# Performance work log

Measured on AMD Instinct MI355X. Metric: run time of the kernel, lower is better.

Reference implementation:

```python
import jax, jax.numpy as jnp
import numpy as np

B, C, D, H, W = 4, 256, 16, 16, 16
INTER = C // 8  # 32


def setup_inputs() -> dict:
    key = jax.random.key(0)
    ks = jax.random.split(key, 8)
    return {
        "x": jax.random.normal(ks[0], (B, C, D, H, W), dtype=jnp.float32),
        "Wq": jax.random.normal(ks[1], (INTER, C), dtype=jnp.float32) * 0.05,
        "bq": jax.random.normal(ks[2], (INTER,), dtype=jnp.float32) * 0.05,
        "Wk": jax.random.normal(ks[3], (INTER, C), dtype=jnp.float32) * 0.05,
        "bk": jax.random.normal(ks[4], (INTER,), dtype=jnp.float32) * 0.05,
        "Wv": jax.random.normal(ks[5], (C, C), dtype=jnp.float32) * 0.05,
        "bv": jax.random.normal(ks[6], (C,), dtype=jnp.float32) * 0.05,
        "gamma": jax.random.normal(ks[7], (1,), dtype=jnp.float32),
    }


def reference(x, Wq, bq, Wk, bk, Wv, bv, gamma):
    b, c, d, h, w = x.shape
    n = d * h * w
    xf = x.reshape(b, c, n)  # [B, C, N]
    # 1x1 Conv3d == pointwise channel projection
    q = jnp.einsum("oc,bcn->bon", Wq, xf) + bq[None, :, None]  # [B, inter, N]
    k = jnp.einsum("oc,bcn->bon", Wk, xf) + bk[None, :, None]  # [B, inter, N]
    v = jnp.einsum("oc,bcn->bon", Wv, xf) + bv[None, :, None]  # [B, C, N]
    scale = float(q.shape[1]) ** 0.5
    # attn[b, i, j] = <q[:, i], k[:, j]>
    attn = jax.nn.softmax(jnp.einsum("bci,bcj->bij", q, k) / scale, axis=-1)
    # out[b, c, i] = sum_j v[b, c, j] * attn[b, i, j]
    out = jnp.einsum("bcj,bij->bci", v, attn).reshape(b, c, d, h, w)
    return gamma[0] * out + x
```

## Files before the change

### kernel.cpp

```cpp
#include <hip/hip_runtime.h>

#define B_ 4
#define C_ 256
#define N_ 4096
#define INTER_ 32

typedef __attribute__((ext_vector_type(8))) short short8;
typedef __attribute__((ext_vector_type(4))) float f32x4;
typedef __attribute__((ext_vector_type(16))) float f32x16;
typedef __attribute__((ext_vector_type(4))) unsigned int u32x4;

#define TILEB 18432
#define NSTG  (8 * TILEB)

static __device__ __forceinline__ unsigned short f2bf(float f) {
    unsigned int u = __builtin_bit_cast(unsigned int, f);
    u += 0x7fff + ((u >> 16) & 1);
    return (unsigned short)(u >> 16);
}

static __device__ __forceinline__ unsigned int cvtpk(float lo, float hi) {
    unsigned int r;
    asm("v_cvt_pk_bf16_f32 %0, %1, %2" : "=v"(r) : "v"(lo), "v"(hi));
    return r;
}

static __device__ __forceinline__ void pl32swap(unsigned int& a, unsigned int& b) {
    asm("v_permlane32_swap_b32 %0, %1" : "+v"(a), "+v"(b));
}

static __device__ __forceinline__ float exp2a(float x) {
    float r;
    asm("v_exp_f32 %0, %1" : "=v"(r) : "v"(x));
    return r;
}

static __device__ __forceinline__ void gload16(const void* g, void* l) {
    __builtin_amdgcn_global_load_lds(
        (const __attribute__((address_space(1))) void*)g,
        (__attribute__((address_space(3))) void*)l, 16, 0, 0);
}

__global__ __launch_bounds__(256) void prep_kernel(
    const float* __restrict__ Wq, const float* __restrict__ Wk,
    const float* __restrict__ Wv, unsigned short* __restrict__ wb)
{
    int i = blockIdx.x * 256 + threadIdx.x;
    int row = i >> 8, col = i & 255;
    float v;
    if (row < 32)      v = Wq[row * 256 + col];
    else if (row < 64) v = Wk[(row - 32) * 256 + col];
    else               v = Wv[(row - 64) * 256 + col];
    wb[i] = f2bf(v);
}

__global__ __launch_bounds__(256) void qkv_kernel(
    const float* __restrict__ x, const unsigned short* __restrict__ wb,
    const float* __restrict__ bq, const float* __restrict__ bk,
    const float* __restrict__ bv,
    unsigned short* __restrict__ qb, unsigned short* __restrict__ kfrag,
    unsigned short* __restrict__ vfrag)
{
    const int tid  = threadIdx.x;
    const int wave = tid >> 6;
    const int lane = tid & 63;
    const int l31  = lane & 31;
    const int h2   = lane >> 5;
    const int b    = blockIdx.x >> 6;
    const int n0   = (blockIdx.x & 63) * 64;

    __shared__ unsigned int xsh[64 * 129];

    {
        const float* xb = x + ((size_t)b * C_ + 64 * wave) * N_ + n0 + lane;
        unsigned int* dst = xsh + (size_t)lane * 129 + 32 * wave;
        #pragma unroll 8
        for (int s = 0; s < 32; ++s) {
            float v0 = xb[(size_t)(2 * s) * N_];
            float v1 = xb[(size_t)(2 * s + 1) * N_];
            dst[s] = (unsigned int)f2bf(v0) | ((unsigned int)f2bf(v1) << 16);
        }
    }
    __syncthreads();

    const float rs = 0.25504183f;

    #pragma unroll
    for (int u = 0; u < 5; ++u) {
        const int unit = wave + 4 * u;
        const int ch = unit >> 1;
        const int ns = unit & 1;
        const int ncol = n0 + 32 * ns + l31;
        const int jt = (n0 >> 5) + ns;

        const float* bias = (ch == 0) ? bq : (ch == 1) ? bk : (bv + (ch - 2) * 32);
        f32x16 acc;
        #pragma unroll
        for (int r = 0; r < 16; ++r)
            acc[r] = bias[(r & 3) + 8 * (r >> 2) + 4 * h2];

        const unsigned short* wrow = wb + ((size_t)(ch * 32 + l31)) * 256 + 8 * h2;
        const unsigned int*   xrow = xsh + (size_t)(32 * ns + l31) * 129 + 4 * h2;

        #pragma unroll
        for (int kk = 0; kk < 16; ++kk) {
            short8 wa = *reinterpret_cast<const short8*>(wrow + 16 * kk);
            short8 xf = *reinterpret_cast<const short8*>(xrow + 8 * kk);
            acc = __builtin_amdgcn_mfma_f32_32x32x16_bf16(wa, xf, acc, 0, 0, 0);
        }

        if (ch == 0) {
            unsigned short* dst = qb + ((size_t)b * N_ + ncol) * 32;
            #pragma unroll
            for (int q = 0; q < 4; ++q) {
                unsigned int w0 = (unsigned int)f2bf(acc[4 * q] * rs)
                                | ((unsigned int)f2bf(acc[4 * q + 1] * rs) << 16);
                unsigned int w1 = (unsigned int)f2bf(acc[4 * q + 2] * rs)
                                | ((unsigned int)f2bf(acc[4 * q + 3] * rs) << 16);
                unsigned int* p = reinterpret_cast<unsigned int*>(dst + 4 * h2 + 8 * q);
                p[0] = w0; p[1] = w1;
            }
        } else if (ch == 1) {
            unsigned short* kt = kfrag + ((size_t)b * 128 + jt) * 1024;
            #pragma unroll
            for (int r = 0; r < 16; ++r) {
                const int co = (r & 3) + 8 * (r >> 2) + 4 * h2;
                const int addr = ((co >> 4) << 9) + ((l31 + 32 * ((co >> 3) & 1)) << 3)
                               + (co & 7);
                kt[addr] = f2bf(acc[r]);
            }
        } else {
            const int g = ch - 2;
            unsigned short* vt_ = vfrag + (((size_t)b * 128 + jt) * 8 + g) * 1024;
            #pragma unroll
            for (int r = 0; r < 16; ++r) {
                const int co = (r & 3) + 8 * (r >> 2) + 4 * h2;
                const int addr = ((l31 >> 4) << 9) + ((co + 32 * ((l31 >> 3) & 1)) << 3)
                               + (l31 & 7);
                vt_[addr] = f2bf(acc[r]);
            }
        }
    }
}

__global__ __launch_bounds__(512) void attn_kernel(
    const unsigned short* __restrict__ qb, const unsigned short* __restrict__ kfrag,
    const unsigned short* __restrict__ vfrag,
    const float* __restrict__ x, const float* __restrict__ gamma,
    float* __restrict__ out)
{
    const int tid  = threadIdx.x;
    const int wave = tid >> 6;
    const int lane = tid & 63;
    const int l31  = lane & 31;
    const int h2   = lane >> 5;
    const int jq   = wave >> 1;
    const int qs   = wave & 1;

    const int bid  = blockIdx.x;
    const int xcd  = bid & 7;
    const int slot = bid >> 3;
    const int b    = xcd >> 1;
    const int ib   = slot * 2 + (xcd & 1);
    const int iq   = ib * 64 + 32 * qs;

    __shared__ char lds[NSTG];
    __shared__ float m_sh[8][32];
    __shared__ float l_sh[8][32];

    const unsigned short* vtb = vfrag + (size_t)b * 128 * 8192;
    const unsigned short* ktb = kfrag + (size_t)b * 128 * 1024;

    char* reg0 = lds + (jq * 2) * TILEB;
    char* reg1 = reg0 + TILEB;

    short8 qf0 = *reinterpret_cast<const short8*>(
        qb + ((size_t)b * N_ + iq + l31) * 32 + 8 * h2);
    short8 qf1 = *reinterpret_cast<const short8*>(
        qb + ((size_t)b * N_ + iq + l31) * 32 + 8 * h2 + 16);

    f32x16 acc[8];
    #pragma unroll
    for (int g = 0; g < 8; ++g)
        #pragma unroll
        for (int r = 0; r < 16; ++r) acc[g][r] = 0.f;

    float m_run = 0.f;
    float l_run = 0.f;
    const f32x16 z16 = {};

    {
        const char* vs = (const char*)(vtb + (size_t)(jq * 32) * 8192);
        const char* ks = (const char*)(ktb + (size_t)(jq * 32) * 1024);
        #pragma unroll
        for (int s2 = 0; s2 < 9; ++s2) {
            const int off = qs * 9216 + s2 * 1024;
            const char* g = (off < 16384) ? (vs + off) : (ks + (off - 16384));
            gload16(g + lane * 16, reg0 + off);
        }
    }
    __syncthreads();

    #pragma unroll 1
    for (int t = 0; t < 32; ++t) {
        char* cur = (t & 1) ? reg1 : reg0;
        char* nxt = (t & 1) ? reg0 : reg1;

        if (t < 31) {
            const int jtg = jq * 32 + t + 1;
            const char* vs = (const char*)(vtb + (size_t)jtg * 8192);
            const char* ks = (const char*)(ktb + (size_t)jtg * 1024);
            #pragma unroll
            for (int s2 = 0; s2 < 9; ++s2) {
                const int off = qs * 9216 + s2 * 1024;
                const char* g = (off < 16384) ? (vs + off) : (ks + (off - 16384));
                gload16(g + lane * 16, nxt + off);
            }
        }

        const char* kt_ = cur + 16384;
        short8 ka0 = *reinterpret_cast<const short8*>(kt_ + lane * 16);
        short8 ka1 = *reinterpret_cast<const short8*>(kt_ + 1024 + lane * 16);
        f32x16 s = __builtin_amdgcn_mfma_f32_32x32x16_bf16(ka0, qf0, z16, 0, 0, 0);
        s = __builtin_amdgcn_mfma_f32_32x32x16_bf16(ka1, qf1, s, 0, 0, 0);

        float a0 = fmaxf(s[0], s[8]),  a1 = fmaxf(s[1], s[9]);
        float a2 = fmaxf(s[2], s[10]), a3 = fmaxf(s[3], s[11]);
        float a4 = fmaxf(s[4], s[12]), a5 = fmaxf(s[5], s[13]);
        float a6 = fmaxf(s[6], s[14]), a7 = fmaxf(s[7], s[15]);
        a0 = fmaxf(a0, a4); a1 = fmaxf(a1, a5); a2 = fmaxf(a2, a6); a3 = fmaxf(a3, a7);
        float smax = fmaxf(fmaxf(a0, a1), fmaxf(a2, a3));

        if (__any(smax > m_run + 8.0f)) {
            float sm2 = fmaxf(smax, __shfl_xor(smax, 32));
            float mnew = fmaxf(m_run, sm2);
            float corr = exp2a(m_run - mnew);
            m_run = mnew;
            l_run *= corr;
            #pragma unroll
            for (int g = 0; g < 8; ++g)
                #pragma unroll
                for (int r = 0; r < 16; ++r) acc[g][r] *= corr;
        }

        float p[16];
        float lsum = 0.f;
        #pragma unroll
        for (int r = 0; r < 16; ++r) { p[r] = exp2a(s[r] - m_run); lsum += p[r]; }
        l_run += lsum;

        unsigned int X0 = cvtpk(p[0],  p[1]),  X1 = cvtpk(p[2],  p[3]);
        unsigned int Y0 = cvtpk(p[4],  p[5]),  Y1 = cvtpk(p[6],  p[7]);
        unsigned int W0 = cvtpk(p[8],  p[9]),  W1 = cvtpk(p[10], p[11]);
        unsigned int V0 = cvtpk(p[12], p[13]), V1 = cvtpk(p[14], p[15]);
        pl32swap(X0, Y0); pl32swap(X1, Y1);
        pl32swap(W0, V0); pl32swap(W1, V1);
        short8 pb0 = __builtin_bit_cast(short8, u32x4{X0, X1, Y0, Y1});
        short8 pb1 = __builtin_bit_cast(short8, u32x4{W0, W1, V0, V1});

        __builtin_amdgcn_s_setprio(1);
        #pragma unroll
        for (int g = 0; g < 8; ++g) {
            short8 va0 = *reinterpret_cast<const short8*>(cur + g * 2048 + lane * 16);
            short8 va1 = *reinterpret_cast<const short8*>(cur + g * 2048 + 1024 + lane * 16);
            acc[g] = __builtin_amdgcn_mfma_f32_32x32x16_bf16(va0, pb0, acc[g], 0, 0, 0);
            acc[g] = __builtin_amdgcn_mfma_f32_32x32x16_bf16(va1, pb1, acc[g], 0, 0, 0);
        }
        __builtin_amdgcn_s_setprio(0);

        __syncthreads();
    }

    float l_tot = l_run + __shfl_xor(l_run, 32);
    if (lane < 32) { m_sh[wave][lane] = m_run; l_sh[wave][lane] = l_tot; }
    __syncthreads();

    float M = -1e30f, L = 0.f;
    #pragma unroll
    for (int w2 = 0; w2 < 4; ++w2) M = fmaxf(M, m_sh[w2 * 2 + qs][l31]);
    #pragma unroll
    for (int w2 = 0; w2 < 4; ++w2)
        L += exp2a(m_sh[w2 * 2 + qs][l31] - M) * l_sh[w2 * 2 + qs][l31];
    const float wgt = exp2a(m_run - M);
    #pragma unroll
    for (int g = 0; g < 8; ++g)
        #pragma unroll
        for (int r = 0; r < 16; ++r) acc[g][r] *= wgt;

    if (jq >= 2) {
        f32x4* Dr = (f32x4*)(lds + ((jq - 2) * 2 + qs) * 32768);
        #pragma unroll
        for (int g = 0; g < 8; ++g)
            #pragma unroll
            for (int r4 = 0; r4 < 4; ++r4) {
                f32x4 tv;
                #pragma unroll
                for (int e = 0; e < 4; ++e) tv[e] = acc[g][4 * r4 + e];
                Dr[(g * 4 + r4) * 64 + lane] = tv;
            }
    }
    __syncthreads();
    if (jq < 2) {
        const f32x4* Dr = (const f32x4*)(lds + (jq * 2 + qs) * 32768);
        #pragma unroll
        for (int g = 0; g < 8; ++g)
            #pragma unroll
            for (int r4 = 0; r4 < 4; ++r4) {
                f32x4 tv = Dr[(g * 4 + r4) * 64 + lane];
                #pragma unroll
                for (int e = 0; e < 4; ++e) acc[g][4 * r4 + e] += tv[e];
            }
    }
    __syncthreads();
    if (jq == 1) {
        f32x4* Dr = (f32x4*)(lds + (2 + qs) * 32768);
        #pragma unroll
        for (int g = 0; g < 8; ++g)
            #pragma unroll
            for (int r4 = 0; r4 < 4; ++r4) {
                f32x4 tv;
                #pragma unroll
                for (int e = 0; e < 4; ++e) tv[e] = acc[g][4 * r4 + e];
                Dr[(g * 4 + r4) * 64 + lane] = tv;
            }
    }
    __syncthreads();
    if (jq == 0) {
        const f32x4* Dr = (const f32x4*)(lds + (2 + qs) * 32768);
        f32x4* Dw = (f32x4*)(lds + qs * 32768);
        #pragma unroll
        for (int g = 0; g < 8; ++g)
            #pragma unroll
            for (int r4 = 0; r4 < 4; ++r4) {
                f32x4 tv = Dr[(g * 4 + r4) * 64 + lane];
                #pragma unroll
                for (int e = 0; e < 4; ++e) tv[e] += acc[g][4 * r4 + e];
                Dw[(g * 4 + r4) * 64 + lane] = tv;
            }
    }
    __syncthreads();

    const float gma  = gamma[0];
    const float invL = 1.f / L;
    const f32x4* Ds = (const f32x4*)(lds + qs * 32768);
    const int i = iq + l31;
    #pragma unroll
    for (int gi = 0; gi < 2; ++gi) {
        const int g = jq * 2 + gi;
        #pragma unroll
        for (int r4 = 0; r4 < 4; ++r4) {
            f32x4 v = Ds[(g * 4 + r4) * 64 + lane];
            #pragma unroll
            for (int e = 0; e < 4; ++e) {
                const int c = 32 * g + e + 8 * r4 + 4 * h2;
                const size_t off = ((size_t)b * C_ + c) * N_ + i;
                out[off] = gma * v[e] * invL + x[off];
            }
        }
    }
}

extern "C" void kernel_launch(void* const* d_in, const int* in_sizes, int n_in,
                              void* d_out, int out_size, void* d_ws, size_t ws_size,
                              hipStream_t stream) {
    const float* x     = (const float*)d_in[0];
    const float* Wq    = (const float*)d_in[1];
    const float* bq    = (const float*)d_in[2];
    const float* Wk    = (const float*)d_in[3];
    const float* bk    = (const float*)d_in[4];
    const float* Wv    = (const float*)d_in[5];
    const float* bv    = (const float*)d_in[6];
    const float* gamma = (const float*)d_in[7];
    float* out = (float*)d_out;

    unsigned short* ws = (unsigned short*)d_ws;
    unsigned short* qb    = ws;
    unsigned short* kfrag = qb + (size_t)B_ * N_ * INTER_;
    unsigned short* vfrag = kfrag + (size_t)B_ * 128 * 1024;
    unsigned short* wb    = vfrag + (size_t)B_ * 128 * 8192;

    prep_kernel<<<dim3(320), 256, 0, stream>>>(Wq, Wk, Wv, wb);
    qkv_kernel<<<dim3(B_ * (N_ / 64)), 256, 0, stream>>>(
        x, wb, bq, bk, bv, qb, kfrag, vfrag);
    attn_kernel<<<dim3(256), 512, 0, stream>>>(
        qb, kfrag, vfrag, x, gamma, out);
}
```

Baseline: 82.22 us.

## Software-pipeline PV MFMA one tile behind QK/softmax with split V/K staging

Restructures the attention loop so the P·V MFMAs for tile t-1 run while the QK scores and softmax for tile t are computed, with the rescale correction deferred by one step. The LDS layout changes so that V and K each get their own double-buffered region per jq group. V is now loaded in the same iteration it is consumed, and K is prefetched one tile ahead. The aim is to hide softmax latency behind matrix work, but V loads now sit closer to their use, which could expose global-load latency.

```diff
diff --git a/kernel.cpp b/kernel.cpp
--- a/kernel.cpp
+++ b/kernel.cpp
@@ -10,8 +10,8 @@
 typedef __attribute__((ext_vector_type(16))) float f32x16;
 typedef __attribute__((ext_vector_type(4))) unsigned int u32x4;
 
-#define TILEB 18432
-#define NSTG  (8 * TILEB)
+#define JQREG 36864
+#define NSTG  (4 * JQREG)
 
 static __device__ __forceinline__ unsigned short f2bf(float f) {
     unsigned int u = __builtin_bit_cast(unsigned int, f);
@@ -171,8 +171,8 @@
     const unsigned short* vtb = vfrag + (size_t)b * 128 * 8192;
     const unsigned short* ktb = kfrag + (size_t)b * 128 * 1024;
 
-    char* reg0 = lds + (jq * 2) * TILEB;
-    char* reg1 = reg0 + TILEB;
+    char* vbase = lds + jq * JQREG;
+    char* kbase = vbase + 32768;
 
     short8 qf0 = *reinterpret_cast<const short8*>(
         qb + ((size_t)b * N_ + iq + l31) * 32 + 8 * h2);
@@ -189,40 +189,65 @@
     float l_run = 0.f;
     const f32x16 z16 = {};
 
-    {
-        const char* vs = (const char*)(vtb + (size_t)(jq * 32) * 8192);
+    short8 pb0p, pb1p;
+    float corrp = 1.0f;
+    bool  resc  = false;
+
+    if (qs == 1) {
         const char* ks = (const char*)(ktb + (size_t)(jq * 32) * 1024);
-        #pragma unroll
-        for (int s2 = 0; s2 < 9; ++s2) {
-            const int off = qs * 9216 + s2 * 1024;
-            const char* g = (off < 16384) ? (vs + off) : (ks + (off - 16384));
-            gload16(g + lane * 16, reg0 + off);
-        }
+        gload16(ks + lane * 16, kbase);
+        gload16(ks + 1024 + lane * 16, kbase + 1024);
     }
     __syncthreads();
 
     #pragma unroll 1
     for (int t = 0; t < 32; ++t) {
-        char* cur = (t & 1) ? reg1 : reg0;
-        char* nxt = (t & 1) ? reg0 : reg1;
-
-        if (t < 31) {
-            const int jtg = jq * 32 + t + 1;
+        const int jtg = jq * 32 + t;
+        char* vw   = vbase + (t & 1) * 16384;
+        char* vprv = vbase + ((t & 1) ^ 1) * 16384;
+        char* kcur = kbase + (t & 1) * 2048;
+
+        {
             const char* vs = (const char*)(vtb + (size_t)jtg * 8192);
-            const char* ks = (const char*)(ktb + (size_t)jtg * 1024);
-            #pragma unroll
-            for (int s2 = 0; s2 < 9; ++s2) {
-                const int off = qs * 9216 + s2 * 1024;
-                const char* g = (off < 16384) ? (vs + off) : (ks + (off - 16384));
-                gload16(g + lane * 16, nxt + off);
-            }
-        }
-
-        const char* kt_ = cur + 16384;
-        short8 ka0 = *reinterpret_cast<const short8*>(kt_ + lane * 16);
-        short8 ka1 = *reinterpret_cast<const short8*>(kt_ + 1024 + lane * 16);
+            if (qs == 0) {
+                #pragma unroll
+                for (int s2 = 0; s2 < 8; ++s2)
+                    gload16(vs + s2 * 1024 + lane * 16, vw + s2 * 1024);
+            } else {
+                #pragma unroll
+                for (int s2 = 8; s2 < 16; ++s2)
+                    gload16(vs + s2 * 1024 + lane * 16, vw + s2 * 1024);
+                if (t < 31) {
+                    const char* ks = (const char*)(ktb + (size_t)(jtg + 1) * 1024);
+                    char* kw = kbase + ((t + 1) & 1) * 2048;
+                    gload16(ks + lane * 16, kw);
+                    gload16(ks + 1024 + lane * 16, kw + 1024);
+                }
+            }
+        }
+
+        short8 ka0 = *reinterpret_cast<const short8*>(kcur + lane * 16);
+        short8 ka1 = *reinterpret_cast<const short8*>(kcur + 1024 + lane * 16);
         f32x16 s = __builtin_amdgcn_mfma_f32_32x32x16_bf16(ka0, qf0, z16, 0, 0, 0);
         s = __builtin_amdgcn_mfma_f32_32x32x16_bf16(ka1, qf1, s, 0, 0, 0);
+
+        if (t > 0) {
+            if (resc) {
+                #pragma unroll
+                for (int g = 0; g < 8; ++g)
+                    #pragma unroll
+                    for (int r = 0; r < 16; ++r) acc[g][r] *= corrp;
+            }
+            __builtin_amdgcn_s_setprio(1);
+            #pragma unroll
+            for (int g = 0; g < 8; ++g) {
+                short8 va0 = *reinterpret_cast<const short8*>(vprv + g * 2048 + lane * 16);
+                short8 va1 = *reinterpret_cast<const short8*>(vprv + g * 2048 + 1024 + lane * 16);
+                acc[g] = __builtin_amdgcn_mfma_f32_32x32x16_bf16(va0, pb0p, acc[g], 0, 0, 0);
+                acc[g] = __builtin_amdgcn_mfma_f32_32x32x16_bf16(va1, pb1p, acc[g], 0, 0, 0);
+            }
+            __builtin_amdgcn_s_setprio(0);
+        }
 
         float a0 = fmaxf(s[0], s[8]),  a1 = fmaxf(s[1], s[9]);
         float a2 = fmaxf(s[2], s[10]), a3 = fmaxf(s[3], s[11]);
@@ -231,16 +256,15 @@
         a0 = fmaxf(a0, a4); a1 = fmaxf(a1, a5); a2 = fmaxf(a2, a6); a3 = fmaxf(a3, a7);
         float smax = fmaxf(fmaxf(a0, a1), fmaxf(a2, a3));
 
-        if (__any(smax > m_run + 8.0f)) {
+        resc = __any(smax > m_run + 8.0f);
+        if (resc) {
             float sm2 = fmaxf(smax, __shfl_xor(smax, 32));
             float mnew = fmaxf(m_run, sm2);
-            float corr = exp2a(m_run - mnew);
+            corrp = exp2a(m_run - mnew);
             m_run = mnew;
-            l_run *= corr;
-            #pragma unroll
-            for (int g = 0; g < 8; ++g)
-                #pragma unroll
-                for (int r = 0; r < 16; ++r) acc[g][r] *= corr;
+            l_run *= corrp;
+        } else {
+            corrp = 1.0f;
         }
 
         float p[16];
@@ -255,20 +279,27 @@
         unsigned int V0 = cvtpk(p[12], p[13]), V1 = cvtpk(p[14], p[15]);
         pl32swap(X0, Y0); pl32swap(X1, Y1);
         pl32swap(W0, V0); pl32swap(W1, V1);
-        short8 pb0 = __builtin_bit_cast(short8, u32x4{X0, X1, Y0, Y1});
-        short8 pb1 = __builtin_bit_cast(short8, u32x4{W0, W1, V0, V1});
-
-        __builtin_amdgcn_s_setprio(1);
+        pb0p = __builtin_bit_cast(short8, u32x4{X0, X1, Y0, Y1});
+        pb1p = __builtin_bit_cast(short8, u32x4{W0, W1, V0, V1});
+
+        __syncthreads();
+    }
+
+    {
+        char* vprv = vbase + 16384;
+        if (resc) {
+            #pragma unroll
+            for (int g = 0; g < 8; ++g)
+                #pragma unroll
+                for (int r = 0; r < 16; ++r) acc[g][r] *= corrp;
+        }
         #pragma unroll
         for (int g = 0; g < 8; ++g) {
-            short8 va0 = *reinterpret_cast<const short8*>(cur + g * 2048 + lane * 16);
-            short8 va1 = *reinterpret_cast<const short8*>(cur + g * 2048 + 1024 + lane * 16);
-            acc[g] = __builtin_amdgcn_mfma_f32_32x32x16_bf16(va0, pb0, acc[g], 0, 0, 0);
-            acc[g] = __builtin_amdgcn_mfma_f32_32x32x16_bf16(va1, pb1, acc[g], 0, 0, 0);
-        }
-        __builtin_amdgcn_s_setprio(0);
-
-        __syncthreads();
+            short8 va0 = *reinterpret_cast<const short8*>(vprv + g * 2048 + lane * 16);
+            short8 va1 = *reinterpret_cast<const short8*>(vprv + g * 2048 + 1024 + lane * 16);
+            acc[g] = __builtin_amdgcn_mfma_f32_32x32x16_bf16(va0, pb0p, acc[g], 0, 0, 0);
+            acc[g] = __builtin_amdgcn_mfma_f32_32x32x16_bf16(va1, pb1p, acc[g], 0, 0, 0);
+        }
     }
 
     float l_tot = l_run + __shfl_xor(l_run, 32);
```

Result: slower. 94.33 us (+14.7%).

## Split attention key range across 2 waves instead of 4 per query tile

Applied to the files above, without the earlier changes.

Halves the attention workgroup from 512 to 256 threads, so each key-split wave group walks 64 key tiles instead of 32. LDS staging shrinks to 4 tiles and the cross-wave reduction becomes a single store/accumulate step, with launch bounds set to allow two blocks per CU. This trades intra-block key parallelism for lower LDS use, less reduction work and possible co-residency of blocks. The cost is a longer serial loop per wave.

```diff
diff --git a/kernel.cpp b/kernel.cpp
--- a/kernel.cpp
+++ b/kernel.cpp
@@ -11,7 +11,7 @@
 typedef __attribute__((ext_vector_type(4))) unsigned int u32x4;
 
 #define TILEB 18432
-#define NSTG  (8 * TILEB)
+#define NSTG  (4 * TILEB)
 
 static __device__ __forceinline__ unsigned short f2bf(float f) {
     unsigned int u = __builtin_bit_cast(unsigned int, f);
@@ -143,7 +143,7 @@
     }
 }
 
-__global__ __launch_bounds__(512) void attn_kernel(
+__global__ __launch_bounds__(256, 2) void attn_kernel(
     const unsigned short* __restrict__ qb, const unsigned short* __restrict__ kfrag,
     const unsigned short* __restrict__ vfrag,
     const float* __restrict__ x, const float* __restrict__ gamma,
@@ -165,8 +165,8 @@
     const int iq   = ib * 64 + 32 * qs;
 
     __shared__ char lds[NSTG];
-    __shared__ float m_sh[8][32];
-    __shared__ float l_sh[8][32];
+    __shared__ float m_sh[4][32];
+    __shared__ float l_sh[4][32];
 
     const unsigned short* vtb = vfrag + (size_t)b * 128 * 8192;
     const unsigned short* ktb = kfrag + (size_t)b * 128 * 1024;
@@ -190,8 +190,8 @@
     const f32x16 z16 = {};
 
     {
-        const char* vs = (const char*)(vtb + (size_t)(jq * 32) * 8192);
-        const char* ks = (const char*)(ktb + (size_t)(jq * 32) * 1024);
+        const char* vs = (const char*)(vtb + (size_t)(jq * 64) * 8192);
+        const char* ks = (const char*)(ktb + (size_t)(jq * 64) * 1024);
         #pragma unroll
         for (int s2 = 0; s2 < 9; ++s2) {
             const int off = qs * 9216 + s2 * 1024;
@@ -202,12 +202,12 @@
     __syncthreads();
 
     #pragma unroll 1
-    for (int t = 0; t < 32; ++t) {
+    for (int t = 0; t < 64; ++t) {
         char* cur = (t & 1) ? reg1 : reg0;
         char* nxt = (t & 1) ? reg0 : reg1;
 
-        if (t < 31) {
-            const int jtg = jq * 32 + t + 1;
+        if (t < 63) {
+            const int jtg = jq * 64 + t + 1;
             const char* vs = (const char*)(vtb + (size_t)jtg * 8192);
             const char* ks = (const char*)(ktb + (size_t)jtg * 1024);
             #pragma unroll
@@ -275,20 +275,19 @@
     if (lane < 32) { m_sh[wave][lane] = m_run; l_sh[wave][lane] = l_tot; }
     __syncthreads();
 
-    float M = -1e30f, L = 0.f;
-    #pragma unroll
-    for (int w2 = 0; w2 < 4; ++w2) M = fmaxf(M, m_sh[w2 * 2 + qs][l31]);
-    #pragma unroll
-    for (int w2 = 0; w2 < 4; ++w2)
-        L += exp2a(m_sh[w2 * 2 + qs][l31] - M) * l_sh[w2 * 2 + qs][l31];
+    const float m0 = m_sh[qs][l31];
+    const float m1 = m_sh[2 + qs][l31];
+    const float M  = fmaxf(m0, m1);
+    const float L  = exp2a(m0 - M) * l_sh[qs][l31]
+                   + exp2a(m1 - M) * l_sh[2 + qs][l31];
     const float wgt = exp2a(m_run - M);
     #pragma unroll
     for (int g = 0; g < 8; ++g)
         #pragma unroll
         for (int r = 0; r < 16; ++r) acc[g][r] *= wgt;
 
-    if (jq >= 2) {
-        f32x4* Dr = (f32x4*)(lds + ((jq - 2) * 2 + qs) * 32768);
+    f32x4* D = reinterpret_cast<f32x4*>(lds);
+    if (jq == 1) {
         #pragma unroll
         for (int g = 0; g < 8; ++g)
             #pragma unroll
@@ -296,60 +295,32 @@
                 f32x4 tv;
                 #pragma unroll
                 for (int e = 0; e < 4; ++e) tv[e] = acc[g][4 * r4 + e];
-                Dr[(g * 4 + r4) * 64 + lane] = tv;
-            }
-    }
-    __syncthreads();
-    if (jq < 2) {
-        const f32x4* Dr = (const f32x4*)(lds + (jq * 2 + qs) * 32768);
+                D[qs * 2048 + (g * 4 + r4) * 64 + lane] = tv;
+            }
+    }
+    __syncthreads();
+    if (jq == 0) {
         #pragma unroll
         for (int g = 0; g < 8; ++g)
             #pragma unroll
             for (int r4 = 0; r4 < 4; ++r4) {
-                f32x4 tv = Dr[(g * 4 + r4) * 64 + lane];
-                #pragma unroll
-                for (int e = 0; e < 4; ++e) acc[g][4 * r4 + e] += tv[e];
-            }
-    }
-    __syncthreads();
-    if (jq == 1) {
-        f32x4* Dr = (f32x4*)(lds + (2 + qs) * 32768);
-        #pragma unroll
-        for (int g = 0; g < 8; ++g)
-            #pragma unroll
-            for (int r4 = 0; r4 < 4; ++r4) {
-                f32x4 tv;
-                #pragma unroll
-                for (int e = 0; e < 4; ++e) tv[e] = acc[g][4 * r4 + e];
-                Dr[(g * 4 + r4) * 64 + lane] = tv;
-            }
-    }
-    __syncthreads();
-    if (jq == 0) {
-        const f32x4* Dr = (const f32x4*)(lds + (2 + qs) * 32768);
-        f32x4* Dw = (f32x4*)(lds + qs * 32768);
-        #pragma unroll
-        for (int g = 0; g < 8; ++g)
-            #pragma unroll
-            for (int r4 = 0; r4 < 4; ++r4) {
-                f32x4 tv = Dr[(g * 4 + r4) * 64 + lane];
+                f32x4 tv = D[qs * 2048 + (g * 4 + r4) * 64 + lane];
                 #pragma unroll
                 for (int e = 0; e < 4; ++e) tv[e] += acc[g][4 * r4 + e];
-                Dw[(g * 4 + r4) * 64 + lane] = tv;
+                D[qs * 2048 + (g * 4 + r4) * 64 + lane] = tv;
             }
     }
     __syncthreads();
 
     const float gma  = gamma[0];
     const float invL = 1.f / L;
-    const f32x4* Ds = (const f32x4*)(lds + qs * 32768);
     const int i = iq + l31;
     #pragma unroll
-    for (int gi = 0; gi < 2; ++gi) {
-        const int g = jq * 2 + gi;
+    for (int gi = 0; gi < 4; ++gi) {
+        const int g = jq * 4 + gi;
         #pragma unroll
         for (int r4 = 0; r4 < 4; ++r4) {
-            f32x4 v = Ds[(g * 4 + r4) * 64 + lane];
+            f32x4 v = D[qs * 2048 + (g * 4 + r4) * 64 + lane];
             #pragma unroll
             for (int e = 0; e < 4; ++e) {
                 const int c = 32 * g + e + 8 * r4 + 4 * h2;
@@ -382,6 +353,6 @@
     prep_kernel<<<dim3(320), 256, 0, stream>>>(Wq, Wk, Wv, wb);
     qkv_kernel<<<dim3(B_ * (N_ / 64)), 256, 0, stream>>>(
         x, wb, bq, bk, bv, qb, kfrag, vfrag);
-    attn_kernel<<<dim3(256), 512, 0, stream>>>(
+    attn_kernel<<<dim3(256), 256, 0, stream>>>(
         qb, kfrag, vfrag, x, gamma, out);
 }
```

Result: slower. 93.77 us (+14.0%).
